# Kernel tuning notes

Measured on AMD Instinct MI355X. Metric: run time of the kernel, lower is better.

## Reference

```python
import jax, jax.numpy as jnp
import numpy as np

H = 1024     # hidden_size
NH = 16      # num heads
HD = H // NH # head_dim = 64
I = 4096     # intermediate_size
EPS = 1e-6


def rmsnorm(x, w, eps=EPS):
    var = jnp.mean(jnp.square(x), axis=-1, keepdims=True)
    return x * jax.lax.rsqrt(var + eps) * w


def attention(x, ctx, wq, wk, wv, wo):
    # x: [B,S,H], ctx: [B,Skv,H]; weights stored [in,out]
    B, S, _ = x.shape
    Skv = ctx.shape[1]
    q = (x @ wq).reshape(B, S, NH, HD)
    k = (ctx @ wk).reshape(B, Skv, NH, HD)
    v = (ctx @ wv).reshape(B, Skv, NH, HD)
    scores = jnp.einsum('bqhd,bkhd->bhqk', q, k) * (HD ** -0.5)
    attn = jax.nn.softmax(scores.astype(jnp.float32), axis=-1).astype(q.dtype)
    out = jnp.einsum('bhqk,bkhd->bqhd', attn, v).reshape(B, S, NH * HD)
    return out @ wo


def mlp(x, wg, wu, wd):
    return (jax.nn.silu(x @ wg) * (x @ wu)) @ wd


def setup_inputs() -> dict:
    key = jax.random.key(0)
    ks = jax.random.split(key, 16)
    p = lambda k, shape: (jax.random.normal(k, shape, jnp.float32) * 0.02)
    return {
        'hidden_states': jax.random.normal(ks[0], (1, 2048, H), jnp.float32),
        'context': jax.random.normal(ks[1], (1, 2048, H), jnp.float32),
        'sa_norm_w': jnp.ones((H,), jnp.float32),
        'sa_wq': p(ks[2], (H, NH * HD)),
        'sa_wk': p(ks[3], (H, NH * HD)),
        'sa_wv': p(ks[4], (H, NH * HD)),
        'sa_wo': p(ks[5], (NH * HD, H)),
        'ca_norm_w': jnp.ones((H,), jnp.float32),
        'ca_wq': p(ks[6], (H, NH * HD)),
        'ca_wk': p(ks[7], (H, NH * HD)),
        'ca_wv': p(ks[8], (H, NH * HD)),
        'ca_wo': p(ks[9], (NH * HD, H)),
        'mlp_norm_w': jnp.ones((H,), jnp.float32),
        'w_gate': p(ks[10], (H, I)),
        'w_up': p(ks[11], (H, I)),
        'w_down': p(ks[12], (I, H)),
    }


def reference(hidden_states, context, sa_norm_w, sa_wq, sa_wk, sa_wv, sa_wo,
              ca_norm_w, ca_wq, ca_wk, ca_wv, ca_wo,
              mlp_norm_w, w_gate, w_up, w_down):
    # self-attention block
    residual = hidden_states
    h = rmsnorm(hidden_states, sa_norm_w)
    h = residual + attention(h, h, sa_wq, sa_wk, sa_wv, sa_wo)
    # cross-attention block
    residual = h
    hn = rmsnorm(h, ca_norm_w)
    h = residual + attention(hn, context, ca_wq, ca_wk, ca_wv, ca_wo)
    # MLP block
    residual = h
    hn = rmsnorm(h, mlp_norm_w)
    h = residual + mlp(hn, w_gate, w_up, w_down)
    return h
```

## Files before the change

kernel.cpp:

```cpp
#include <hip/hip_runtime.h>

#define H 1024
#define S 2048
#define NH 16
#define HD 64
#define ISZ 4096

typedef __attribute__((ext_vector_type(8))) short s8v;
typedef __attribute__((ext_vector_type(4))) short s4v;
typedef __attribute__((ext_vector_type(4))) float f4v;

__device__ __forceinline__ short f2bf(float f) {
    unsigned u = __builtin_bit_cast(unsigned, f);
    unsigned r = (u + 0x7FFFu + ((u >> 16) & 1u)) >> 16;
    return (short)r;
}
__device__ __forceinline__ float bf2f(short s) {
    unsigned u = ((unsigned)(unsigned short)s) << 16;
    return __builtin_bit_cast(float, u);
}

__device__ __forceinline__ void gload_lds16(const short* g, short* l) {
    __builtin_amdgcn_global_load_lds(
        (const __attribute__((address_space(1))) void*)g,
        (__attribute__((address_space(3))) void*)l, 16, 0, 0);
}

struct PreArgs {
    const void* hid; const void* ctx;
    const void* sanw; const void* canw; const void* mlpnw;
    const void* w[11];
    short* hidc; short* ctxc; short* xn;
    short* canw_o; short* mlpnw_o;
    short* wT[11];
    int* flag_out;
};

__device__ __forceinline__ void tr_tile(const void* src, short* dst, int K, int N,
                                        int k0, int n0, int rmul, int roff,
                                        int isbf, float* tile ) {
    int t = threadIdx.x;
    int c = t & 31, r0 = t >> 5;
    if (isbf) {
        const short* s = (const short*)src;
#pragma unroll
        for (int i = 0; i < 4; i++)
            tile[(r0 + i * 8) * 33 + c] = bf2f(s[(k0 + r0 + i * 8) * N + n0 + c]);
    } else {
        const float* s = (const float*)src;
#pragma unroll
        for (int i = 0; i < 4; i++)
            tile[(r0 + i * 8) * 33 + c] = s[(k0 + r0 + i * 8) * N + n0 + c];
    }
    __syncthreads();
#pragma unroll
    for (int i = 0; i < 4; i++)
        dst[((n0 + r0 + i * 8) * rmul + roff) * K + k0 + c] = f2bf(tile[c * 33 + r0 + i * 8]);
}

__global__ __launch_bounds__(256) void preamble_kernel(PreArgs pa) {
    __shared__ float tile[32 * 33];
    __shared__ float red[4];
    int b = blockIdx.x;
    int t = threadIdx.x;
    int isbf = (((const unsigned*)pa.sanw)[0] == 0x3F803F80u);
    if (blockIdx.x == 0 && t == 0) pa.flag_out[0] = isbf;

    if (b < 2048) {
        int row = b;
        float xf[4];
        if (isbf) {
            s4v xv = *(const s4v*)((const short*)pa.hid + row * H + t * 4);
#pragma unroll
            for (int j = 0; j < 4; j++) xf[j] = bf2f(xv[j]);
        } else {
            const float* s = (const float*)pa.hid + row * H + t * 4;
#pragma unroll
            for (int j = 0; j < 4; j++) xf[j] = s[j];
        }
        float ss = 0.f;
        s4v cv;
#pragma unroll
        for (int j = 0; j < 4; j++) { cv[j] = f2bf(xf[j]); xf[j] = bf2f(cv[j]); ss += xf[j] * xf[j]; }
        *(s4v*)(pa.hidc + row * H + t * 4) = cv;
        int lane = t & 63, wid = t >> 6;
#pragma unroll
        for (int off = 32; off >= 1; off >>= 1) ss += __shfl_xor(ss, off);
        if (lane == 0) red[wid] = ss;
        __syncthreads();
        float tot = red[0] + red[1] + red[2] + red[3];
        float scale = rsqrtf(tot * (1.f / (float)H) + 1e-6f);
        float wv[4];
        if (isbf) {
            s4v wq = *(const s4v*)((const short*)pa.sanw + t * 4);
#pragma unroll
            for (int j = 0; j < 4; j++) wv[j] = bf2f(wq[j]);
        } else {
            const float* s = (const float*)pa.sanw + t * 4;
#pragma unroll
            for (int j = 0; j < 4; j++) wv[j] = s[j];
        }
        s4v ov;
#pragma unroll
        for (int j = 0; j < 4; j++) ov[j] = f2bf(xf[j] * scale * wv[j]);
        *(s4v*)(pa.xn + row * H + t * 4) = ov;
        return;
    }
    b -= 2048;
    if (b < 1024) {
        int i8 = b * 2048 + t * 8;
        if (isbf) {
            *(s8v*)(pa.ctxc + i8) = *(const s8v*)((const short*)pa.ctx + i8);
        } else {
            const float* s = (const float*)pa.ctx;
            s8v o;
#pragma unroll
            for (int j = 0; j < 8; j++) o[j] = f2bf(s[i8 + j]);
            *(s8v*)(pa.ctxc + i8) = o;
        }
        return;
    }
    b -= 1024;
    if (b < 2) {
        const void* src = (b == 0) ? pa.canw : pa.mlpnw;
        short* dst = (b == 0) ? pa.canw_o : pa.mlpnw_o;
        if (isbf) { if (t * 4 < H) *(s4v*)(dst + t * 4) = *(const s4v*)((const short*)src + t * 4); }
        else {
            const float* s = (const float*)src;
            s4v o;
#pragma unroll
            for (int j = 0; j < 4; j++) o[j] = f2bf(s[t * 4 + j]);
            *(s4v*)(dst + t * 4) = o;
        }
        return;
    }
    b -= 2;
    if (b < 8 * 1024) {
        int w = b >> 10, tl = b & 1023;
        tr_tile(pa.w[w], pa.wT[w], H, H, (tl & 31) * 32, (tl >> 5) * 32, 1, 0, isbf, tile);
        return;
    }
    b -= 8 * 1024;
    if (b < 2 * 4096) {
        int w = 8 + (b >> 12), tl = b & 4095;
        tr_tile(pa.w[w], pa.wT[8], H, ISZ, (tl & 31) * 32, (tl >> 5) * 32, 2, w - 8, isbf, tile);
        return;
    }
    b -= 2 * 4096;
    {
        tr_tile(pa.w[10], pa.wT[10], ISZ, H, (b & 127) * 32, (b >> 7) * 32, 1, 0, isbf, tile);
    }
}

__global__ __launch_bounds__(256) void rmsnorm_kernel(const short* __restrict__ x,
                                                      const short* __restrict__ w,
                                                      short* __restrict__ out) {
    int row = blockIdx.x;
    int t = threadIdx.x;
    int lane = t & 63, wid = t >> 6;
    const short* xr = x + row * H;

    s4v xv = *(const s4v*)(xr + t * 4);
    float xf[4];
    float ss = 0.f;
#pragma unroll
    for (int j = 0; j < 4; j++) { xf[j] = bf2f(xv[j]); ss += xf[j] * xf[j]; }
#pragma unroll
    for (int off = 32; off >= 1; off >>= 1) ss += __shfl_xor(ss, off);

    __shared__ float red[4];
    if (lane == 0) red[wid] = ss;
    __syncthreads();
    float tot = red[0] + red[1] + red[2] + red[3];
    float scale = rsqrtf(tot * (1.f / (float)H) + 1e-6f);

    s4v wv = *(const s4v*)(w + t * 4);
    s4v ov;
#pragma unroll
    for (int j = 0; j < 4; j++) ov[j] = f2bf(xf[j] * scale * bf2f(wv[j]));
    *(s4v*)(out + row * H + t * 4) = ov;
}

template <int BM_, int BN_>
__global__ __launch_bounds__(256, 2) void gemm_bt_kernel(
    const short* __restrict__ A0, const short* __restrict__ A1, int split, int lda,
    const short* __restrict__ Bt,
    void* __restrict__ C, int ldc, int K,
    const short* __restrict__ res,
    const int* __restrict__ dtype_flag,
    short* __restrict__ vtbuf, int vcol0,
    short* __restrict__ silu_out) {

    constexpr int MC = BM_ / 32;
    constexpr int NC = BN_ / 32;

    const short* A = (blockIdx.y < split) ? A0 : A1;
    int m0 = blockIdx.x * BM_;
    int n0 = blockIdx.y * BN_;

    __shared__ short As[2 * BM_ * 32];
    __shared__ short Bs[2 * BN_ * 32];

    int t = threadIdx.x;
    int lane = t & 63, wid = t >> 6;
    int quad = lane >> 4, l15 = lane & 15;
    int wr = wid >> 1, wc = wid & 1;

    f4v acc[MC][NC] = {};

    int ld4 = lane >> 2, lc8 = (lane & 3) * 8;

    for (int k0 = 0; k0 < K; k0 += 64) {
#pragma unroll
        for (int h = 0; h < 2; h++) {
#pragma unroll
            for (int i = 0; i < BM_ / 64; i++)
                gload_lds16(A + (m0 + wid * (BM_ / 4) + i * 16 + ld4) * lda + k0 + h * 32 + lc8,
                            As + h * BM_ * 32 + (wid * (BM_ / 4) + i * 16) * 32);
#pragma unroll
            for (int i = 0; i < BN_ / 64; i++)
                gload_lds16(Bt + (n0 + wid * (BN_ / 4) + i * 16 + ld4) * K + k0 + h * 32 + lc8,
                            Bs + h * BN_ * 32 + (wid * (BN_ / 4) + i * 16) * 32);
        }
        __syncthreads();

#pragma unroll
        for (int h = 0; h < 2; h++) {
            s8v af[MC], bfv[NC];
#pragma unroll
            for (int mc = 0; mc < MC; mc++)
                af[mc] = *(const s8v*)(As + h * BM_ * 32 + (wr * (BM_ / 2) + mc * 16 + l15) * 32 + quad * 8);
#pragma unroll
            for (int nc = 0; nc < NC; nc++)
                bfv[nc] = *(const s8v*)(Bs + h * BN_ * 32 + (wc * (BN_ / 2) + nc * 16 + l15) * 32 + quad * 8);

#pragma unroll
            for (int mc = 0; mc < MC; mc++)
#pragma unroll
                for (int nc = 0; nc < NC; nc++)
                    acc[mc][nc] = __builtin_amdgcn_mfma_f32_16x16x32_bf16(af[mc], bfv[nc], acc[mc][nc], 0, 0, 0);
        }
        __syncthreads();
    }

    if (silu_out) {
#pragma unroll
        for (int mc = 0; mc < MC; mc++) {
#pragma unroll
            for (int nc = 0; nc < NC; nc++) {
                int row = m0 + wr * (BM_ / 2) + mc * 16 + quad * 4;
                int col = n0 + wc * (BN_ / 2) + nc * 16 + l15;
#pragma unroll
                for (int r = 0; r < 4; r++) {
                    float v = acc[mc][nc][r];
                    float other = __shfl_xor(v, 1);
                    if ((l15 & 1) == 0) {
                        float sig = 1.f / (1.f + __expf(-v));
                        silu_out[(row + r) * ISZ + (col >> 1)] = f2bf(v * sig * other);
                    }
                }
            }
        }
        return;
    }

    int out_fp32 = (dtype_flag != nullptr) && (dtype_flag[0] == 0);

#pragma unroll
    for (int mc = 0; mc < MC; mc++) {
#pragma unroll
        for (int nc = 0; nc < NC; nc++) {
            int row = m0 + wr * (BM_ / 2) + mc * 16 + quad * 4;
            int col = n0 + wc * (BN_ / 2) + nc * 16 + l15;
#pragma unroll
            for (int r = 0; r < 4; r++) {
                float vf = acc[mc][nc][r];
                if (res) vf += bf2f(res[(row + r) * ldc + col]);
                if (vtbuf && col >= vcol0)
                    vtbuf[(col - vcol0) * S + row + r] = f2bf(vf);
                else if (out_fp32)
                    ((float*)C)[(row + r) * ldc + col] = vf;
                else
                    ((short*)C)[(row + r) * ldc + col] = f2bf(vf);
            }
        }
    }
}

__global__ __launch_bounds__(256) void flash_attn_kernel(const short* __restrict__ q,
                                                         const short* __restrict__ k,
                                                         const short* __restrict__ vt,
                                                         int rs,
                                                         short* __restrict__ o) {
    int h = blockIdx.y;
    int q0 = blockIdx.x * 64;
    int t = threadIdx.x;
    int lane = t & 63, wid = t >> 6;
    int quad = lane >> 4, l15 = lane & 15;

    __shared__ short K2[2 * 128 * 32];
    __shared__ short V2[4 * 64 * 32];
    __shared__ short Pw[4][2048];

    int ld4 = lane >> 2, lc8 = (lane & 3) * 8;

    s8v bq[2];
    int qrow = q0 + wid * 16 + l15;
#pragma unroll
    for (int c = 0; c < 2; c++) {
        s8v raw = *(const s8v*)(q + qrow * rs + h * HD + c * 32 + quad * 8);
#pragma unroll
        for (int j = 0; j < 8; j++) bq[c][j] = f2bf(0.125f * bf2f(raw[j]));
    }

    f4v o_acc[4] = {};
    float m_s = -INFINITY, l_s = 0.f;

    for (int kv0 = 0; kv0 < S; kv0 += 128) {
#pragma unroll
        for (int dc = 0; dc < 2; dc++)
#pragma unroll
            for (int i = 0; i < 2; i++)
                gload_lds16(k + (kv0 + wid * 32 + i * 16 + ld4) * rs + h * HD + dc * 32 + lc8,
                            K2 + dc * 4096 + (wid * 32 + i * 16) * 32);
#pragma unroll
        for (int kc2 = 0; kc2 < 4; kc2++)
            gload_lds16(vt + (h * HD + wid * 16 + ld4) * S + kv0 + kc2 * 32 + lc8,
                        V2 + kc2 * 2048 + (wid * 16) * 32);
        __syncthreads();

        f4v st[8];
#pragma unroll
        for (int kc = 0; kc < 8; kc++) {
            f4v a_ = (f4v){0.f, 0.f, 0.f, 0.f};
#pragma unroll
            for (int dc = 0; dc < 2; dc++) {
                s8v kf = *(const s8v*)(K2 + dc * 4096 + (kc * 16 + l15) * 32 + quad * 8);
                a_ = __builtin_amdgcn_mfma_f32_16x16x32_bf16(kf, bq[dc], a_, 0, 0, 0);
            }
            st[kc] = a_;
        }

        float mloc = -INFINITY;
#pragma unroll
        for (int kc = 0; kc < 8; kc++)
#pragma unroll
            for (int r = 0; r < 4; r++) mloc = fmaxf(mloc, st[kc][r]);
        mloc = fmaxf(mloc, __shfl_xor(mloc, 16));
        mloc = fmaxf(mloc, __shfl_xor(mloc, 32));
        float m_new = fmaxf(m_s, mloc);
        float alpha = __expf(m_s - m_new);
        float lloc = 0.f;
#pragma unroll
        for (int kc = 0; kc < 8; kc++)
#pragma unroll
            for (int r = 0; r < 4; r++) {
                float p = __expf(st[kc][r] - m_new);
                st[kc][r] = p;
                lloc += p;
            }
        lloc += __shfl_xor(lloc, 16);
        lloc += __shfl_xor(lloc, 32);
        l_s = l_s * alpha + lloc;
        m_s = m_new;
#pragma unroll
        for (int nd = 0; nd < 4; nd++)
#pragma unroll
            for (int r = 0; r < 4; r++) o_acc[nd][r] *= alpha;

#pragma unroll
        for (int kc = 0; kc < 8; kc++)
#pragma unroll
            for (int r = 0; r < 4; r++)
                Pw[wid][(kc >> 1) * 512 + l15 * 32 + (kc & 1) * 16 + quad * 4 + r] = f2bf(st[kc][r]);

#pragma unroll
        for (int nd = 0; nd < 4; nd++) {
#pragma unroll
            for (int kc2 = 0; kc2 < 4; kc2++) {
                s8v vf = *(const s8v*)(V2 + kc2 * 2048 + (nd * 16 + l15) * 32 + quad * 8);
                s8v pf = *(const s8v*)(Pw[wid] + kc2 * 512 + l15 * 32 + quad * 8);
                o_acc[nd] = __builtin_amdgcn_mfma_f32_16x16x32_bf16(vf, pf, o_acc[nd], 0, 0, 0);
            }
        }
        __syncthreads();
    }

    float inv = 1.f / l_s;
#pragma unroll
    for (int nd = 0; nd < 4; nd++)
#pragma unroll
        for (int r = 0; r < 4; r++)
            Pw[wid][l15 * 64 + nd * 16 + quad * 4 + r] = f2bf(o_acc[nd][r] * inv);

    int qr = lane >> 2, dc2 = (lane & 3) * 16;
    s8v x0 = *(const s8v*)(Pw[wid] + qr * 64 + dc2);
    s8v x1 = *(const s8v*)(Pw[wid] + qr * 64 + dc2 + 8);
    short* dst = o + (q0 + wid * 16 + qr) * H + h * HD + dc2;
    *(s8v*)(dst) = x0;
    *(s8v*)(dst + 8) = x1;
}

extern "C" void kernel_launch(void* const* d_in, const int* in_sizes, int n_in,
                              void* d_out, int out_size, void* d_ws, size_t ws_size,
                              hipStream_t stream) {
    const int SH = S * H;
    const int WH = H * H;
    const int WI = H * ISZ;

    int* flag = (int*)d_ws;
    short* base = (short*)d_ws + 16;

    short* hidc   = base;
    short* ctxc   = hidc + SH;
    short* sanw   = ctxc + SH;
    short* canw   = sanw + H;
    short* mlpnw  = canw + H;
    short* saqkvT = mlpnw + H;
    short* sawoT  = saqkvT + 3 * WH;
    short* caqkvT = sawoT + WH;
    short* cawoT  = caqkvT + 3 * WH;
    short* wguT   = cawoT + WH;
    short* wdT    = wguT + 2 * WI;
    short* xn     = wdT + WI;
    short* qkv    = xn + SH;
    short* ao     = qkv + 3 * SH;
    short* h1     = ao + SH;
    short* gu     = qkv;
    short* h2     = qkv + 8 * SH;
    short* vt     = h2 + SH;

    dim3 blk(256);

    PreArgs pa;
    pa.hid = d_in[0]; pa.ctx = d_in[1];
    pa.sanw = d_in[2]; pa.canw = d_in[7]; pa.mlpnw = d_in[12];
    const void* wsrc[11] = {d_in[3], d_in[4], d_in[5], d_in[6],
                            d_in[8], d_in[9], d_in[10], d_in[11],
                            d_in[13], d_in[14], d_in[15]};
    short* wdst[11] = {saqkvT, saqkvT + WH, saqkvT + 2 * WH, sawoT,
                       caqkvT, caqkvT + WH, caqkvT + 2 * WH, cawoT,
                       wguT, wguT , wdT};
    for (int i = 0; i < 11; i++) { pa.w[i] = wsrc[i]; pa.wT[i] = wdst[i]; }
    pa.hidc = hidc; pa.ctxc = ctxc; pa.xn = xn;
    pa.canw_o = canw; pa.mlpnw_o = mlpnw;
    pa.flag_out = flag;
    const int pre_blocks = 2048 + 1024 + 2 + 8 * 1024 + 2 * 4096 + 4096;
    preamble_kernel<<<pre_blocks, blk, 0, stream>>>(pa);

    gemm_bt_kernel<64, 128><<<dim3(S / 64, 3 * H / 128), blk, 0, stream>>>(
        xn, xn, 24, H, saqkvT, qkv, 3 * H, H, nullptr, nullptr, vt, 2 * H, nullptr);
    flash_attn_kernel<<<dim3(S / 64, NH), blk, 0, stream>>>(qkv, qkv + H, vt, 3 * H, ao);
    gemm_bt_kernel<64, 64><<<dim3(S / 64, H / 64), blk, 0, stream>>>(
        ao, ao, 16, H, sawoT, h1, H, H, hidc, nullptr, nullptr, 0, nullptr);

    rmsnorm_kernel<<<S, blk, 0, stream>>>(h1, canw, xn);
    gemm_bt_kernel<64, 128><<<dim3(S / 64, 3 * H / 128), blk, 0, stream>>>(
        xn, ctxc, 8, H, caqkvT, qkv, 3 * H, H, nullptr, nullptr, vt, 2 * H, nullptr);
    flash_attn_kernel<<<dim3(S / 64, NH), blk, 0, stream>>>(qkv, qkv + H, vt, 3 * H, ao);
    gemm_bt_kernel<64, 64><<<dim3(S / 64, H / 64), blk, 0, stream>>>(
        ao, ao, 16, H, cawoT, h2, H, H, h1, nullptr, nullptr, 0, nullptr);

    rmsnorm_kernel<<<S, blk, 0, stream>>>(h2, mlpnw, xn);
    gemm_bt_kernel<128, 128><<<dim3(S / 128, 2 * ISZ / 128), blk, 0, stream>>>(
        xn, xn, 64, H, wguT, nullptr, 2 * ISZ, H, nullptr, nullptr, nullptr, 0, gu);
    gemm_bt_kernel<64, 64><<<dim3(S / 64, H / 64), blk, 0, stream>>>(
        gu, gu, 16, ISZ, wdT, d_out, H, ISZ, h2, flag, nullptr, 0, nullptr);
}
```

Measured before the change: 498.8 us.

## Fold RMSNorm into adjacent GEMMs via gamma-scaled weights and row sum-of-squares

Removes the two standalone rmsnorm kernels. The norm gammas for the cross-attention Q and MLP gate/up weights are folded into the transposed weights during the preamble. The o-proj GEMM epilogues accumulate per-row sums of squares with atomics, and the next GEMM applies rsqrt scaling to its accumulators. This saves two launches and a read/write of the normalized activations, at the cost of float atomics, an extra rsqrt per output element, and rounding differences from scaling after the bf16 matmul.

```diff
diff --git a/kernel.cpp b/kernel.cpp
--- a/kernel.cpp
+++ b/kernel.cpp
@@ -31,14 +31,14 @@
     const void* sanw; const void* canw; const void* mlpnw;
     const void* w[11];
     short* hidc; short* ctxc; short* xn;
-    short* canw_o; short* mlpnw_o;
     short* wT[11];
+    float* rowss;
     int* flag_out;
 };
 
 __device__ __forceinline__ void tr_tile(const void* src, short* dst, int K, int N,
                                         int k0, int n0, int rmul, int roff,
-                                        int isbf, float* tile ) {
+                                        int isbf, const void* gamma, float* tile) {
     int t = threadIdx.x;
     int c = t & 31, r0 = t >> 5;
     if (isbf) {
@@ -52,10 +52,13 @@
         for (int i = 0; i < 4; i++)
             tile[(r0 + i * 8) * 33 + c] = s[(k0 + r0 + i * 8) * N + n0 + c];
     }
+    float gval = 1.f;
+    if (gamma)
+        gval = isbf ? bf2f(((const short*)gamma)[k0 + c]) : ((const float*)gamma)[k0 + c];
     __syncthreads();
 #pragma unroll
     for (int i = 0; i < 4; i++)
-        dst[((n0 + r0 + i * 8) * rmul + roff) * K + k0 + c] = f2bf(tile[c * 33 + r0 + i * 8]);
+        dst[((n0 + r0 + i * 8) * rmul + roff) * K + k0 + c] = f2bf(tile[c * 33 + r0 + i * 8] * gval);
 }
 
 __global__ __launch_bounds__(256) void preamble_kernel(PreArgs pa) {
@@ -122,63 +125,28 @@
     }
     b -= 1024;
     if (b < 2) {
-        const void* src = (b == 0) ? pa.canw : pa.mlpnw;
-        short* dst = (b == 0) ? pa.canw_o : pa.mlpnw_o;
-        if (isbf) { if (t * 4 < H) *(s4v*)(dst + t * 4) = *(const s4v*)((const short*)src + t * 4); }
-        else {
-            const float* s = (const float*)src;
-            s4v o;
-#pragma unroll
-            for (int j = 0; j < 4; j++) o[j] = f2bf(s[t * 4 + j]);
-            *(s4v*)(dst + t * 4) = o;
-        }
+        f4v z = (f4v){0.f, 0.f, 0.f, 0.f};
+        *(f4v*)(pa.rowss + b * 2048 + t * 8) = z;
+        *(f4v*)(pa.rowss + b * 2048 + t * 8 + 4) = z;
         return;
     }
     b -= 2;
     if (b < 8 * 1024) {
         int w = b >> 10, tl = b & 1023;
-        tr_tile(pa.w[w], pa.wT[w], H, H, (tl & 31) * 32, (tl >> 5) * 32, 1, 0, isbf, tile);
+        const void* g = (w == 4) ? pa.canw : nullptr;
+        tr_tile(pa.w[w], pa.wT[w], H, H, (tl & 31) * 32, (tl >> 5) * 32, 1, 0, isbf, g, tile);
         return;
     }
     b -= 8 * 1024;
     if (b < 2 * 4096) {
         int w = 8 + (b >> 12), tl = b & 4095;
-        tr_tile(pa.w[w], pa.wT[8], H, ISZ, (tl & 31) * 32, (tl >> 5) * 32, 2, w - 8, isbf, tile);
+        tr_tile(pa.w[w], pa.wT[8], H, ISZ, (tl & 31) * 32, (tl >> 5) * 32, 2, w - 8, isbf, pa.mlpnw, tile);
         return;
     }
     b -= 2 * 4096;
     {
-        tr_tile(pa.w[10], pa.wT[10], ISZ, H, (b & 127) * 32, (b >> 7) * 32, 1, 0, isbf, tile);
-    }
-}
-
-__global__ __launch_bounds__(256) void rmsnorm_kernel(const short* __restrict__ x,
-                                                      const short* __restrict__ w,
-                                                      short* __restrict__ out) {
-    int row = blockIdx.x;
-    int t = threadIdx.x;
-    int lane = t & 63, wid = t >> 6;
-    const short* xr = x + row * H;
-
-    s4v xv = *(const s4v*)(xr + t * 4);
-    float xf[4];
-    float ss = 0.f;
-#pragma unroll
-    for (int j = 0; j < 4; j++) { xf[j] = bf2f(xv[j]); ss += xf[j] * xf[j]; }
-#pragma unroll
-    for (int off = 32; off >= 1; off >>= 1) ss += __shfl_xor(ss, off);
-
-    __shared__ float red[4];
-    if (lane == 0) red[wid] = ss;
-    __syncthreads();
-    float tot = red[0] + red[1] + red[2] + red[3];
-    float scale = rsqrtf(tot * (1.f / (float)H) + 1e-6f);
-
-    s4v wv = *(const s4v*)(w + t * 4);
-    s4v ov;
-#pragma unroll
-    for (int j = 0; j < 4; j++) ov[j] = f2bf(xf[j] * scale * bf2f(wv[j]));
-    *(s4v*)(out + row * H + t * 4) = ov;
+        tr_tile(pa.w[10], pa.wT[10], ISZ, H, (b & 127) * 32, (b >> 7) * 32, 1, 0, isbf, nullptr, tile);
+    }
 }
 
 template <int BM_, int BN_>
@@ -189,7 +157,8 @@
     const short* __restrict__ res,
     const int* __restrict__ dtype_flag,
     short* __restrict__ vtbuf, int vcol0,
-    short* __restrict__ silu_out) {
+    short* __restrict__ silu_out,
+    const float* __restrict__ scaleA, float* __restrict__ ssout) {
 
     constexpr int MC = BM_ / 32;
     constexpr int NC = BN_ / 32;
@@ -243,6 +212,8 @@
         __syncthreads();
     }
 
+    bool do_scale = (scaleA != nullptr) && ((int)blockIdx.y < split);
+
     if (silu_out) {
 #pragma unroll
         for (int mc = 0; mc < MC; mc++) {
@@ -253,6 +224,7 @@
 #pragma unroll
                 for (int r = 0; r < 4; r++) {
                     float v = acc[mc][nc][r];
+                    if (do_scale) v *= rsqrtf(scaleA[row + r] * (1.f / 1024.f) + 1e-6f);
                     float other = __shfl_xor(v, 1);
                     if ((l15 & 1) == 0) {
                         float sig = 1.f / (1.f + __expf(-v));
@@ -265,6 +237,7 @@
     }
 
     int out_fp32 = (dtype_flag != nullptr) && (dtype_flag[0] == 0);
+    float sq[MC][4] = {};
 
 #pragma unroll
     for (int mc = 0; mc < MC; mc++) {
@@ -275,7 +248,9 @@
 #pragma unroll
             for (int r = 0; r < 4; r++) {
                 float vf = acc[mc][nc][r];
+                if (do_scale) vf *= rsqrtf(scaleA[row + r] * (1.f / 1024.f) + 1e-6f);
                 if (res) vf += bf2f(res[(row + r) * ldc + col]);
+                if (ssout) sq[mc][r] += vf * vf;
                 if (vtbuf && col >= vcol0)
                     vtbuf[(col - vcol0) * S + row + r] = f2bf(vf);
                 else if (out_fp32)
@@ -284,6 +259,21 @@
                     ((short*)C)[(row + r) * ldc + col] = f2bf(vf);
             }
         }
+    }
+
+    if (ssout) {
+#pragma unroll
+        for (int mc = 0; mc < MC; mc++)
+#pragma unroll
+            for (int r = 0; r < 4; r++) {
+                float v = sq[mc][r];
+                v += __shfl_xor(v, 1);
+                v += __shfl_xor(v, 2);
+                v += __shfl_xor(v, 4);
+                v += __shfl_xor(v, 8);
+                if (l15 == 0)
+                    atomicAdd(&ssout[m0 + wr * (BM_ / 2) + mc * 16 + quad * 4 + r], v);
+            }
     }
 }
 
@@ -413,10 +403,7 @@
 
     short* hidc   = base;
     short* ctxc   = hidc + SH;
-    short* sanw   = ctxc + SH;
-    short* canw   = sanw + H;
-    short* mlpnw  = canw + H;
-    short* saqkvT = mlpnw + H;
+    short* saqkvT = ctxc + SH;
     short* sawoT  = saqkvT + 3 * WH;
     short* caqkvT = sawoT + WH;
     short* cawoT  = caqkvT + 3 * WH;
@@ -429,6 +416,8 @@
     short* gu     = qkv;
     short* h2     = qkv + 8 * SH;
     short* vt     = h2 + SH;
+    float* rowss1 = (float*)(vt + SH);
+    float* rowss2 = rowss1 + S;
 
     dim3 blk(256);
 
@@ -443,27 +432,31 @@
                        wguT, wguT , wdT};
     for (int i = 0; i < 11; i++) { pa.w[i] = wsrc[i]; pa.wT[i] = wdst[i]; }
     pa.hidc = hidc; pa.ctxc = ctxc; pa.xn = xn;
-    pa.canw_o = canw; pa.mlpnw_o = mlpnw;
+    pa.rowss = rowss1;
     pa.flag_out = flag;
     const int pre_blocks = 2048 + 1024 + 2 + 8 * 1024 + 2 * 4096 + 4096;
     preamble_kernel<<<pre_blocks, blk, 0, stream>>>(pa);
 
     gemm_bt_kernel<64, 128><<<dim3(S / 64, 3 * H / 128), blk, 0, stream>>>(
-        xn, xn, 24, H, saqkvT, qkv, 3 * H, H, nullptr, nullptr, vt, 2 * H, nullptr);
+        xn, xn, 24, H, saqkvT, qkv, 3 * H, H, nullptr, nullptr, vt, 2 * H, nullptr,
+        nullptr, nullptr);
     flash_attn_kernel<<<dim3(S / 64, NH), blk, 0, stream>>>(qkv, qkv + H, vt, 3 * H, ao);
     gemm_bt_kernel<64, 64><<<dim3(S / 64, H / 64), blk, 0, stream>>>(
-        ao, ao, 16, H, sawoT, h1, H, H, hidc, nullptr, nullptr, 0, nullptr);
-
-    rmsnorm_kernel<<<S, blk, 0, stream>>>(h1, canw, xn);
+        ao, ao, 16, H, sawoT, h1, H, H, hidc, nullptr, nullptr, 0, nullptr,
+        nullptr, rowss1);
+
     gemm_bt_kernel<64, 128><<<dim3(S / 64, 3 * H / 128), blk, 0, stream>>>(
-        xn, ctxc, 8, H, caqkvT, qkv, 3 * H, H, nullptr, nullptr, vt, 2 * H, nullptr);
+        h1, ctxc, 8, H, caqkvT, qkv, 3 * H, H, nullptr, nullptr, vt, 2 * H, nullptr,
+        rowss1, nullptr);
     flash_attn_kernel<<<dim3(S / 64, NH), blk, 0, stream>>>(qkv, qkv + H, vt, 3 * H, ao);
     gemm_bt_kernel<64, 64><<<dim3(S / 64, H / 64), blk, 0, stream>>>(
-        ao, ao, 16, H, cawoT, h2, H, H, h1, nullptr, nullptr, 0, nullptr);
-
-    rmsnorm_kernel<<<S, blk, 0, stream>>>(h2, mlpnw, xn);
+        ao, ao, 16, H, cawoT, h2, H, H, h1, nullptr, nullptr, 0, nullptr,
+        nullptr, rowss2);
+
     gemm_bt_kernel<128, 128><<<dim3(S / 128, 2 * ISZ / 128), blk, 0, stream>>>(
-        xn, xn, 64, H, wguT, nullptr, 2 * ISZ, H, nullptr, nullptr, nullptr, 0, gu);
+        h2, h2, 64, H, wguT, nullptr, 2 * ISZ, H, nullptr, nullptr, nullptr, 0, gu,
+        rowss2, nullptr);
     gemm_bt_kernel<64, 64><<<dim3(S / 64, H / 64), blk, 0, stream>>>(
-        gu, gu, 16, ISZ, wdT, d_out, H, ISZ, h2, flag, nullptr, 0, nullptr);
-}
+        gu, gu, 16, ISZ, wdT, d_out, H, ISZ, h2, flag, nullptr, 0, nullptr,
+        nullptr, nullptr);
+}
```

New measurement: 513.1 us. 2.9% more time.
